# Performance work log

Measured on AMD Instinct MI355X. Metric: run time of the kernel, lower is better.

## Reference

```python
import math
import jax, jax.numpy as jnp
import numpy as np

B, N, DIM, H = 2, 4096, 1024, 16
DH = DIM // H
LEVELS = int(math.log2(N))
SCALE = 1.0 / math.sqrt(DH)


def build_lookup_table(seq_len):
    """Replicates build_hierarchical_index_lookup_table (numpy, static)."""
    levels = int(math.log2(seq_len))
    total_nodes = 2 * seq_len - 1
    max_valid = total_nodes - 2
    idx = np.full((seq_len, levels), -1, dtype=np.int32)
    cm = np.zeros((seq_len, levels), dtype=bool)
    for n in range(seq_len):
        nc = n
        for l in range(levels):
            if l == 0:
                pair = nc
                nn = nc ^ 1
            else:
                pair = nc // 2 + seq_len
                nn = pair ^ 1  # (nc//2 + seq_len) ^ 1 per Python precedence
            if nn > max_valid:
                break
            if pair < nn:
                cm[n, l] = True  # neighbor is to the right -> causally masked
            idx[n, l] = nn
            nc = nn
    return idx, cm


def setup_inputs() -> dict:
    key = jax.random.key(0)
    ks = jax.random.split(key, 12)
    w = lambda k: (jax.random.normal(k, (DIM, DIM), dtype=jnp.float32) * 0.02)
    idx_np, cm_np = build_lookup_table(N)
    return {
        "x": jax.random.normal(ks[0], (B, N, DIM), dtype=jnp.float32),
        "Wq_y": w(ks[1]), "Wk_y": w(ks[2]), "Wv_y": w(ks[3]),
        "Wo_y": w(ks[4]), "bo_y": jnp.zeros((DIM,), jnp.float32),
        "Wq_x": w(ks[5]), "Wk_x": w(ks[6]), "Wv_x": w(ks[7]),
        "Wo_x": w(ks[8]), "bo_x": jnp.zeros((DIM,), jnp.float32),
        "idx_map": jnp.asarray(idx_np, dtype=jnp.int32),       # [N, LEVELS]
        "causal_mask": jnp.asarray(cm_np, dtype=jnp.bool_),    # [N, LEVELS]
    }


def _heads(t):
    b, n, _ = t.shape
    return t.reshape(b, n, H, DH)


def _forward(x, Wq_y, Wk_y, Wv_y, Wo_y, bo_y, Wq_x, Wk_x, Wv_x, Wo_x, bo_x,
             idx_map, causal_mask):
    # ---- stage 1: build parent nodes level by level (online 2-child softmax merge)
    nodes = [x]  # leaves: [B, N, DIM]; parents appended level by level
    cur = x
    for _ in range(LEVELS):
        pre = 0.5 * (cur[:, 0::2] + cur[:, 1::2])     # parent query source [B,P,DIM]
        q = _heads(pre @ Wq_y)                        # [B,P,H,DH]
        k = _heads(cur @ Wk_y)                        # [B,C,H,DH]
        v = _heads(cur @ Wv_y)
        s0 = jnp.einsum('bphd,bphd->bph', q, k[:, 0::2]) * SCALE
        s1 = jnp.einsum('bphd,bphd->bph', q, k[:, 1::2]) * SCALE
        m = jnp.maximum(s0, s1)
        e0 = jnp.exp(s0 - m)
        e1 = jnp.exp(s1 - m)
        denom = e0 + e1 + 1e-9
        parent = ((e0 / denom)[..., None] * v[:, 0::2]
                  + (e1 / denom)[..., None] * v[:, 1::2])   # [B,P,H,DH]
        bp, pp = parent.shape[0], parent.shape[1]
        parent = parent.reshape(bp, pp, DIM) @ Wo_y + bo_y
        nodes.append(parent)
        cur = parent
    h_all = jnp.concatenate(nodes, axis=1)            # [B, 2N-1, DIM]

    # ---- stage 2: fused multi-level gather attention over self + neighbors
    Q = _heads(x @ Wq_x)                              # leaf queries [B,N,H,DH]
    K_all = _heads(h_all @ Wk_x)                      # [B,2N-1,H,DH]
    V_all = _heads(h_all @ Wv_x)

    k_cross = jnp.take(K_all, idx_map, axis=1)        # [B,N,LEVELS,H,DH]
    v_cross = jnp.take(V_all, idx_map, axis=1)

    s_self = jnp.einsum('bnhd,bnhd->bnh', Q, K_all[:, :N]) * SCALE   # [B,N,H]
    s_cross = jnp.einsum('bnhd,bnlhd->bnhl', Q, k_cross) * SCALE     # [B,N,H,L]
    neg_inf = jnp.float32(-jnp.inf)
    s_cross = jnp.where(causal_mask[None, :, None, :], neg_inf, s_cross)

    scores = jnp.concatenate([s_self[..., None], s_cross], axis=-1)  # [B,N,H,L+1]
    w = jax.nn.softmax(scores, axis=-1)
    out = (w[..., 0:1] * V_all[:, :N]
           + jnp.einsum('bnhl,bnlhd->bnhd', w[..., 1:], v_cross))    # [B,N,H,DH]
    return out.reshape(B, N, DIM) @ Wo_x + bo_x


def reference(x, Wq_y, Wk_y, Wv_y, Wo_y, bo_y, Wq_x, Wk_x, Wv_x, Wo_x, bo_x,
              idx_map, causal_mask):
    return _forward(x, Wq_y, Wk_y, Wv_y, Wo_y, bo_y,
                    Wq_x, Wk_x, Wv_x, Wo_x, bo_x, idx_map, causal_mask)
```

## Files before the change

### kernel.cpp

```cpp
#include <hip/hip_runtime.h>
#include <stdint.h>

#define H_NODES 8191
#define NN 4096
#define DIMC 1024

typedef __bf16 bf16x8 __attribute__((ext_vector_type(8)));
typedef float f32x4 __attribute__((ext_vector_type(4)));

__device__ __forceinline__ float b2f(ushort u) {
  union { uint32_t i; float f; } x; x.i = ((uint32_t)u) << 16; return x.f;
}
__device__ __forceinline__ ushort f2b(float f) {
  union { float f; uint32_t i; } x; x.f = f;
  uint32_t r = x.i + 0x7FFFu + ((x.i >> 16) & 1u);
  return (ushort)(r >> 16);
}
__device__ __forceinline__ void load16f(const ushort* p, float* f) {
  const uint32_t* w = (const uint32_t*)p;
  #pragma unroll
  for (int i = 0; i < 8; ++i) {
    uint32_t v = w[i];
    f[2 * i]     = b2f((ushort)(v & 0xffff));
    f[2 * i + 1] = b2f((ushort)(v >> 16));
  }
}
__device__ __forceinline__ void store16b(ushort* p, const float* f) {
  uint32_t w[8];
  #pragma unroll
  for (int i = 0; i < 8; ++i)
    w[i] = (uint32_t)f2b(f[2 * i]) | ((uint32_t)f2b(f[2 * i + 1]) << 16);
  *(uint4*)p = *(const uint4*)&w[0];
  *(uint4*)(p + 8) = *(const uint4*)&w[4];
}

struct WPtrs { const float* w[8]; };

__global__ void __launch_bounds__(256) transpose_w_k(WPtrs wp, ushort* __restrict__ dst) {
  __shared__ float t[32][33];
  const float* src = wp.w[blockIdx.z];
  int c0 = blockIdx.x * 32, r0 = blockIdx.y * 32;
  int tx = threadIdx.x, ty = threadIdx.y;
  #pragma unroll
  for (int i = ty; i < 32; i += 8)
    t[i][tx] = src[(long)(r0 + i) * DIMC + c0 + tx];
  __syncthreads();
  ushort* d = dst + (long)blockIdx.z * DIMC * DIMC;
  #pragma unroll
  for (int i = ty; i < 32; i += 8)
    d[(long)(c0 + i) * DIMC + r0 + tx] = f2b(t[tx][i]);
}

__global__ void __launch_bounds__(256) cvt_x_k(const float* __restrict__ x, ushort* __restrict__ h) {
  long t = (long)blockIdx.x * 256 + threadIdx.x;
  long i = t << 2;
  if (i >= (long)2 * NN * DIMC) return;
  long row = i >> 10;
  int col = (int)(i & 1023);
  long b = row >> 12;
  long n = row & 4095;
  float4 v = *(const float4*)(x + i);
  ushort* d = h + ((b * H_NODES + n) << 10) + col;
  uint2 pk;
  pk.x = (uint32_t)f2b(v.x) | ((uint32_t)f2b(v.y) << 16);
  pk.y = (uint32_t)f2b(v.z) | ((uint32_t)f2b(v.w) << 16);
  *(uint2*)d = pk;
}

__global__ void __launch_bounds__(256) avg_pairs_k(const ushort* __restrict__ h,
    ushort* __restrict__ pre, int P, int offL) {
  long t = (long)blockIdx.x * 256 + threadIdx.x;
  if (t >= (long)2 * P * 128) return;
  int dblk = (int)(t & 127);
  long r = t >> 7;
  int b = (r >= P) ? 1 : 0;
  int p = (int)(r - (long)b * P);
  const ushort* c = h + (((long)(b * H_NODES + offL + 2 * p)) << 10) + dblk * 8;
  const uint4 a0 = *(const uint4*)c;
  const uint4 a1 = *(const uint4*)(c + DIMC);
  const uint32_t* pa = (const uint32_t*)&a0;
  const uint32_t* pb = (const uint32_t*)&a1;
  uint32_t outw[4];
  #pragma unroll
  for (int i = 0; i < 4; ++i) {
    float x0 = b2f((ushort)(pa[i] & 0xffff)), x1 = b2f((ushort)(pa[i] >> 16));
    float y0 = b2f((ushort)(pb[i] & 0xffff)), y1 = b2f((ushort)(pb[i] >> 16));
    ushort r0 = f2b(0.5f * (x0 + y0)), r1 = f2b(0.5f * (x1 + y1));
    outw[i] = (uint32_t)r0 | ((uint32_t)r1 << 16);
  }
  *(uint4*)(pre + (((long)(b * P + p)) << 10) + dblk * 8) = *(const uint4*)outw;
}

struct GemmDesc {
  const ushort* A; long sAb;
  const ushort* Bt;
  const float* bias;
  void* C; long sCb; int ldc;
  int M; int outMode;
  int tX, tY;
  ushort* preC;
  long sPreB;
};

__device__ __forceinline__ void stage_tile(const GemmDesc& d, const ushort* Ab,
    int row0, int col0, ushort* lA, ushort* lB, int kt, int wave, int lane) {
  #pragma unroll
  for (int j = 0; j < 2; ++j) {
    int s = wave * 128 + j * 64 + lane;
    int r = s >> 2;
    int g = (s & 3) ^ ((r >> 1) & 3);
    int gr = row0 + r; gr = (gr < d.M) ? gr : (d.M - 1);
    const ushort* srcA = Ab + (long)gr * DIMC + kt * 32 + g * 8;
    __builtin_amdgcn_global_load_lds(
        (const __attribute__((address_space(1))) void*)(uintptr_t)srcA,
        (__attribute__((address_space(3))) void*)(uint32_t)(uintptr_t)(lA + (wave * 128 + j * 64) * 8),
        16, 0, 0);
    const ushort* srcB = d.Bt + (long)(col0 + r) * DIMC + kt * 32 + g * 8;
    __builtin_amdgcn_global_load_lds(
        (const __attribute__((address_space(1))) void*)(uintptr_t)srcB,
        (__attribute__((address_space(3))) void*)(uint32_t)(uintptr_t)(lB + (wave * 128 + j * 64) * 8),
        16, 0, 0);
  }
}

__device__ __forceinline__ void gemm_tile(const GemmDesc& d, int bz, int row0, int col0,
    ushort (*lA)[4096], ushort (*lB)[4096], int tid) {
  const ushort* Ab = d.A + (long)bz * d.sAb;
  int wave = tid >> 6, lane = tid & 63;
  int wr = wave >> 1, wc = wave & 1;

  f32x4 acc[4][4];
  #pragma unroll
  for (int m = 0; m < 4; ++m)
    #pragma unroll
    for (int n = 0; n < 4; ++n) acc[m][n] = (f32x4){0.f, 0.f, 0.f, 0.f};

  stage_tile(d, Ab, row0, col0, lA[0], lB[0], 0, wave, lane);
  stage_tile(d, Ab, row0, col0, lA[1], lB[1], 1, wave, lane);
  asm volatile("s_waitcnt vmcnt(4)" ::: "memory");
  __builtin_amdgcn_s_barrier();

  int rr = lane & 15, g4 = lane >> 4;
  for (int kt = 0; kt < 32; ++kt) {
    int cur = kt % 3;
    if (kt + 2 < 32)
      stage_tile(d, Ab, row0, col0, lA[(kt + 2) % 3], lB[(kt + 2) % 3], kt + 2, wave, lane);
    bf16x8 af[4], bfr[4];
    #pragma unroll
    for (int m = 0; m < 4; ++m) {
      int r = wr * 64 + m * 16 + rr;
      int slot = g4 ^ ((r >> 1) & 3);
      af[m] = *reinterpret_cast<const bf16x8*>(&lA[cur][r * 32 + slot * 8]);
    }
    #pragma unroll
    for (int n = 0; n < 4; ++n) {
      int r = wc * 64 + n * 16 + rr;
      int slot = g4 ^ ((r >> 1) & 3);
      bfr[n] = *reinterpret_cast<const bf16x8*>(&lB[cur][r * 32 + slot * 8]);
    }
    __builtin_amdgcn_s_setprio(1);
    #pragma unroll
    for (int m = 0; m < 4; ++m)
      #pragma unroll
      for (int n = 0; n < 4; ++n)
        acc[m][n] = __builtin_amdgcn_mfma_f32_16x16x32_bf16(af[m], bfr[n], acc[m][n], 0, 0, 0);
    __builtin_amdgcn_s_setprio(0);
    if (kt < 30) { asm volatile("s_waitcnt vmcnt(4)" ::: "memory"); }
    else         { asm volatile("s_waitcnt vmcnt(0)" ::: "memory"); }
    if (kt < 31) __builtin_amdgcn_s_barrier();
  }

  int rq = lane >> 4;
  #pragma unroll
  for (int n = 0; n < 4; ++n) {
    int col = col0 + wc * 64 + n * 16 + rr;
    float bv = d.bias ? d.bias[col] : 0.0f;
    #pragma unroll
    for (int m = 0; m < 4; ++m) {
      int gr0 = row0 + wr * 64 + m * 16 + rq * 4;
      float vv[4];
      #pragma unroll
      for (int r = 0; r < 4; ++r) vv[r] = acc[m][n][r] + bv;
      #pragma unroll
      for (int r = 0; r < 4; ++r) {
        int gr = gr0 + r;
        if (gr < d.M) {
          long o = (long)bz * d.sCb + (long)gr * d.ldc + col;
          if (d.outMode == 2) ((float*)d.C)[o] = vv[r];
          else ((ushort*)d.C)[o] = f2b(vv[r]);
        }
      }
      if (d.preC) {
        #pragma unroll
        for (int r = 0; r < 4; r += 2) {
          int gr = gr0 + r;
          if (gr + 1 < d.M)
            d.preC[(long)bz * d.sPreB + (long)(gr >> 1) * DIMC + col] =
                f2b(0.5f * (vv[r] + vv[r + 1]));
        }
      }
    }
  }
}

__global__ void __launch_bounds__(256) gemm_multi(GemmDesc d0, GemmDesc d1, int t0) {
  __shared__ __align__(16) ushort lA[3][4096];
  __shared__ __align__(16) ushort lB[3][4096];
  int t = blockIdx.x;
  const GemmDesc& d = (t < t0) ? d0 : d1;
  int u = (t < t0) ? t : t - t0;
  int per = d.tX * d.tY;
  int bz = u / per;
  int rem = u - bz * per;
  int ty = rem / d.tX;
  int tx = rem - ty * d.tX;
  gemm_tile(d, bz, tx * 128, ty * 128, lA, lB, threadIdx.x);
}

__global__ void __launch_bounds__(256) merge_y2_k(const ushort* __restrict__ q,
    const ushort* __restrict__ kv, ushort* __restrict__ outp, int P) {
  int wave = threadIdx.x >> 6, lane = threadIdx.x & 63;
  long w = (long)blockIdx.x * 4 + wave;
  if (w >= (long)2 * P) return;
  int b = (w >= P) ? 1 : 0;
  int p = (int)(w - (long)b * P);
  const ushort* qp = q + (((long)(b * P + p)) << 10) + lane * 16;
  const ushort* kvb = kv + ((long)(b * 2 * P + 2 * p)) * 2048;
  float qf[16], k0f[16], k1f[16];
  load16f(qp, qf);
  load16f(kvb + lane * 16, k0f);
  load16f(kvb + 2048 + lane * 16, k1f);
  float d0 = 0.f, d1 = 0.f;
  #pragma unroll
  for (int j = 0; j < 16; ++j) { d0 += qf[j] * k0f[j]; d1 += qf[j] * k1f[j]; }
  d0 += __shfl_xor(d0, 1); d0 += __shfl_xor(d0, 2);
  d1 += __shfl_xor(d1, 1); d1 += __shfl_xor(d1, 2);
  float s0 = d0 * 0.125f, s1 = d1 * 0.125f;
  float mm = fmaxf(s0, s1);
  float e0 = expf(s0 - mm), e1 = expf(s1 - mm);
  float inv = 1.0f / (e0 + e1 + 1e-9f);
  float w0 = e0 * inv, w1 = e1 * inv;
  float v0f[16], v1f[16], ov[16];
  load16f(kvb + 1024 + lane * 16, v0f);
  load16f(kvb + 2048 + 1024 + lane * 16, v1f);
  #pragma unroll
  for (int j = 0; j < 16; ++j) ov[j] = w0 * v0f[j] + w1 * v1f[j];
  store16b(outp + (((long)(b * P + p)) << 10) + lane * 16, ov);
}

__global__ void __launch_bounds__(256) attn_x2_k(const ushort* __restrict__ Q,
    const ushort* __restrict__ KV, ushort* __restrict__ outp) {
  int wave = threadIdx.x >> 6, lane = threadIdx.x & 63;
  long w = (long)blockIdx.x * 4 + wave;
  int n = (int)(w & 4095);
  int b = (int)(w >> 12);
  const ushort* KVb = KV + (long)b * H_NODES * 2048;
  float qf[16];
  load16f(Q + (((long)b * NN + n) << 10) + lane * 16, qf);
  int nb[13];
  nb[0] = n;
  #pragma unroll
  for (int l = 0; l < 12; ++l) nb[1 + l] = (8192 - (8192 >> l)) + ((n >> l) ^ 1);
  float s[13];
  #pragma unroll
  for (int i = 0; i < 13; ++i) {
    float kf[16];
    load16f(KVb + (long)nb[i] * 2048 + lane * 16, kf);
    float d = 0.f;
    #pragma unroll
    for (int j = 0; j < 16; ++j) d += qf[j] * kf[j];
    d += __shfl_xor(d, 1);
    d += __shfl_xor(d, 2);
    s[i] = d * 0.125f;
  }
  #pragma unroll
  for (int l = 0; l < 12; ++l)
    if (((n >> l) & 1) == 0) s[1 + l] = -__builtin_inff();
  float mm = s[0];
  #pragma unroll
  for (int i = 1; i < 13; ++i) mm = fmaxf(mm, s[i]);
  float e[13], sum = 0.f;
  #pragma unroll
  for (int i = 0; i < 13; ++i) { e[i] = expf(s[i] - mm); sum += e[i]; }
  float inv = 1.0f / sum;
  float ov[16];
  #pragma unroll
  for (int j = 0; j < 16; ++j) ov[j] = 0.f;
  #pragma unroll
  for (int i = 0; i < 13; ++i) {
    float wgt = e[i] * inv;
    float vf[16];
    load16f(KVb + (long)nb[i] * 2048 + 1024 + lane * 16, vf);
    #pragma unroll
    for (int j = 0; j < 16; ++j) ov[j] += wgt * vf[j];
  }
  store16b(outp + (((long)b * NN + n) << 10) + lane * 16, ov);
}

extern "C" void kernel_launch(void* const* d_in, const int* in_sizes, int n_in,
                              void* d_out, int out_size, void* d_ws, size_t ws_size,
                              hipStream_t stream) {
  const float* x    = (const float*)d_in[0];
  const float* Wq_y = (const float*)d_in[1];
  const float* Wk_y = (const float*)d_in[2];
  const float* Wv_y = (const float*)d_in[3];
  const float* Wo_y = (const float*)d_in[4];
  const float* bo_y = (const float*)d_in[5];
  const float* Wq_x = (const float*)d_in[6];
  const float* Wk_x = (const float*)d_in[7];
  const float* Wv_x = (const float*)d_in[8];
  const float* Wo_x = (const float*)d_in[9];
  const float* bo_x = (const float*)d_in[10];

  ushort* wt  = (ushort*)d_ws;
  ushort* h   = wt + (size_t)8 * 1024 * 1024;
  ushort* reg = h + (size_t)2 * H_NODES * DIMC;
  ushort* Qx   = reg;
  ushort* KVa  = Qx + (size_t)2 * 4096 * DIMC;
  ushort* aout = KVa + (size_t)2 * H_NODES * 2048;
  ushort* preB = reg;
  ushort* qbB  = preB + (size_t)2 * 2048 * DIMC;
  ushort* kv1B = qbB + (size_t)2 * 2048 * DIMC;
  ushort* mrgB = kv1B + (size_t)2 * 4096 * 2048;
  ushort* preS = aout;
  ushort* qbS  = preS + (size_t)2 * 256 * DIMC;
  ushort* kv1S = qbS + (size_t)2 * 256 * DIMC;
  ushort* mrgS = kv1S + (size_t)2 * 512 * 2048;

  size_t need = ((size_t)8 * 1024 * 1024 + (size_t)2 * H_NODES * DIMC +
                 (size_t)2 * 4096 * DIMC + (size_t)2 * H_NODES * 2048 +
                 (size_t)2 * 4096 * DIMC) * 2;
  if (ws_size < need) return;

  WPtrs wp;
  wp.w[0] = Wq_y; wp.w[1] = Wk_y; wp.w[2] = Wv_y; wp.w[3] = Wo_y;
  wp.w[4] = Wq_x; wp.w[5] = Wk_x; wp.w[6] = Wv_x; wp.w[7] = Wo_x;
  transpose_w_k<<<dim3(32, 32, 8), dim3(32, 8), 0, stream>>>(wp, wt);
  cvt_x_k<<<8192, 256, 0, stream>>>(x, h);
  avg_pairs_k<<<(2 * 2048 * 128 + 255) / 256, 256, 0, stream>>>(h, preB, 2048, 0);

  auto mk128 = [](const ushort* A, long sAb, const ushort* Bt, const float* bias,
                  void* C, long sCb, int ldc, int M, int outMode, int tY) {
    GemmDesc d; d.A = A; d.sAb = sAb; d.Bt = Bt; d.bias = bias; d.C = C; d.sCb = sCb;
    d.ldc = ldc; d.M = M; d.outMode = outMode; d.tX = (M + 127) / 128; d.tY = tY;
    d.preC = nullptr; d.sPreB = 0;
    return d;
  };
  auto kvSub = [&](long start, int len) {
    return mk128(h + start * DIMC, (long)H_NODES * DIMC, wt + (size_t)5 * 1024 * 1024,
                 nullptr, KVa + start * 2048, (long)H_NODES * 2048, 2048, len, 0, 16);
  };

  for (int l = 0; l < 12; ++l) {
    int P = NN >> (l + 1);
    int offL = 8192 - (8192 >> l);
    int offP = 8192 - (8192 >> (l + 1));
    bool small = (l >= 3);
    ushort* pre = small ? preS : preB;
    ushort* qb  = small ? qbS  : qbB;
    ushort* kv1 = small ? kv1S : kv1B;
    ushort* mrg = small ? mrgS : mrgB;

    GemmDesc dq  = mk128(pre, (long)P * DIMC, wt, nullptr,
                         qb, (long)P * DIMC, DIMC, P, 0, 8);
    GemmDesc dkv = mk128(h + (long)offL * DIMC, (long)H_NODES * DIMC,
                         wt + (size_t)1 * 1024 * 1024, nullptr,
                         kv1, (long)2 * P * 2048, 2048, 2 * P, 0, 16);
    int t0 = dq.tX * dq.tY * 2;
    gemm_multi<<<t0 + dkv.tX * dkv.tY * 2, 256, 0, stream>>>(dq, dkv, t0);

    merge_y2_k<<<(2 * P + 3) / 4, 256, 0, stream>>>(qb, kv1, mrg, P);

    GemmDesc dgo = mk128(mrg, (long)P * DIMC, wt + (size_t)3 * 1024 * 1024, bo_y,
                         h + (long)offP * DIMC, (long)H_NODES * DIMC, DIMC, P, 1, 8);
    if (l < 11) {
      dgo.preC = (l >= 2) ? preS : preB;
      dgo.sPreB = (long)(P / 2) * DIMC;
    }
    GemmDesc att = dgo; int nAtt = 0;
    if (l == 4)      { att = kvSub(0, 2048); }
    else if (l == 5) { att = kvSub(2048, 2048); }
    else if (l == 6) { att = kvSub(4096, 2048); }
    else if (l == 7) { att = kvSub(6144, 1792); }
    else if (l == 8) { att = kvSub(7936, 240); }
    else if (l == 9) { att = mk128(h, (long)H_NODES * DIMC, wt + (size_t)4 * 1024 * 1024,
                                   nullptr, Qx, (long)4096 * DIMC, DIMC, 4096, 0, 8); }
    else if (l == 10) { att = kvSub(8176, 12); }
    else if (l == 11) { att = kvSub(8188, 2); }
    if (l >= 4) nAtt = att.tX * att.tY * 2;
    int n0 = dgo.tX * dgo.tY * 2;
    gemm_multi<<<n0 + nAtt, 256, 0, stream>>>(dgo, att, n0);
  }

  {
    GemmDesc att = kvSub(8190, 1);
    gemm_multi<<<att.tX * att.tY * 2, 256, 0, stream>>>(att, att, att.tX * att.tY * 2);
  }
  attn_x2_k<<<2048, 256, 0, stream>>>(Qx, KVa, aout);
  {
    GemmDesc dox = mk128(aout, (long)4096 * DIMC, wt + (size_t)7 * 1024 * 1024, bo_x,
                         d_out, (long)4096 * DIMC, DIMC, 4096, 2, 8);
    gemm_multi<<<dox.tX * dox.tY * 2, 256, 0, stream>>>(dox, dox, dox.tX * dox.tY * 2);
  }
}
```

Before: 661.3 us.

## Redistribute attention K/V and Q projection GEMMs across more level launches

```diff
diff --git a/kernel.cpp b/kernel.cpp
--- a/kernel.cpp
+++ b/kernel.cpp
@@ -203,12 +203,13 @@
   }
 }
 
-__global__ void __launch_bounds__(256) gemm_multi(GemmDesc d0, GemmDesc d1, int t0) {
+__global__ void __launch_bounds__(256) gemm_multi(GemmDesc d0, GemmDesc d1, GemmDesc d2,
+                                                  int t0, int t1) {
   __shared__ __align__(16) ushort lA[3][4096];
   __shared__ __align__(16) ushort lB[3][4096];
   int t = blockIdx.x;
-  const GemmDesc& d = (t < t0) ? d0 : d1;
-  int u = (t < t0) ? t : t - t0;
+  const GemmDesc& d = (t < t0) ? d0 : ((t < t1) ? d1 : d2);
+  int u = (t < t0) ? t : ((t < t1) ? t - t0 : t - t1);
   int per = d.tX * d.tY;
   int bz = u / per;
   int rem = u - bz * per;
@@ -350,6 +351,9 @@
     return mk128(h + start * DIMC, (long)H_NODES * DIMC, wt + (size_t)5 * 1024 * 1024,
                  nullptr, KVa + start * 2048, (long)H_NODES * 2048, 2048, len, 0, 16);
   };
+  auto tiles = [](const GemmDesc& d) { return d.tX * d.tY * 2; };
+  GemmDesc dQat = mk128(h, (long)H_NODES * DIMC, wt + (size_t)4 * 1024 * 1024, nullptr,
+                        Qx, (long)4096 * DIMC, DIMC, 4096, 0, 8);
 
   for (int l = 0; l < 12; ++l) {
     int P = NN >> (l + 1);
@@ -366,8 +370,18 @@
     GemmDesc dkv = mk128(h + (long)offL * DIMC, (long)H_NODES * DIMC,
                          wt + (size_t)1 * 1024 * 1024, nullptr,
                          kv1, (long)2 * P * 2048, 2048, 2 * P, 0, 16);
-    int t0 = dq.tX * dq.tY * 2;
-    gemm_multi<<<t0 + dkv.tX * dkv.tY * 2, 256, 0, stream>>>(dq, dkv, t0);
+    GemmDesc aq = dkv; int naq = 0;
+    if      (l == 4)  { aq = kvSub(1024, 1024); }
+    else if (l == 5)  { aq = kvSub(4096, 1024); }
+    else if (l == 6)  { aq = kvSub(6144, 1024); }
+    else if (l == 7)  { aq = kvSub(8128, 32); }
+    else if (l == 8)  { aq = kvSub(8160, 16); }
+    else if (l == 9)  { aq = kvSub(8176, 8); }
+    else if (l == 10) { aq = kvSub(8184, 4); }
+    else if (l == 11) { aq = kvSub(8188, 2); }
+    if (l >= 4) naq = tiles(aq);
+    int nq = tiles(dq), nkv = tiles(dkv);
+    gemm_multi<<<nq + nkv + naq, 256, 0, stream>>>(dq, dkv, aq, nq, nq + nkv);
 
     merge_y2_k<<<(2 * P + 3) / 4, 256, 0, stream>>>(qb, kv1, mrg, P);
 
@@ -377,29 +391,27 @@
       dgo.preC = (l >= 2) ? preS : preB;
       dgo.sPreB = (long)(P / 2) * DIMC;
     }
-    GemmDesc att = dgo; int nAtt = 0;
-    if (l == 4)      { att = kvSub(0, 2048); }
-    else if (l == 5) { att = kvSub(2048, 2048); }
-    else if (l == 6) { att = kvSub(4096, 2048); }
-    else if (l == 7) { att = kvSub(6144, 1792); }
-    else if (l == 8) { att = kvSub(7936, 240); }
-    else if (l == 9) { att = mk128(h, (long)H_NODES * DIMC, wt + (size_t)4 * 1024 * 1024,
-                                   nullptr, Qx, (long)4096 * DIMC, DIMC, 4096, 0, 8); }
-    else if (l == 10) { att = kvSub(8176, 12); }
-    else if (l == 11) { att = kvSub(8188, 2); }
-    if (l >= 4) nAtt = att.tX * att.tY * 2;
-    int n0 = dgo.tX * dgo.tY * 2;
-    gemm_multi<<<n0 + nAtt, 256, 0, stream>>>(dgo, att, n0);
+    GemmDesc a1 = dgo, a2 = dgo; int n1 = 0, n2 = 0;
+    if      (l == 3) { a1 = kvSub(0, 1024); n1 = tiles(a1); }
+    else if (l == 4) { a1 = kvSub(2048, 1024); a2 = kvSub(3072, 1024);
+                       n1 = tiles(a1); n2 = tiles(a2); }
+    else if (l == 5) { a1 = dQat; a2 = kvSub(5120, 1024);
+                       n1 = tiles(a1); n2 = tiles(a2); }
+    else if (l == 6) { a1 = kvSub(7168, 960); n1 = tiles(a1); }
+    int n0 = tiles(dgo);
+    gemm_multi<<<n0 + n1 + n2, 256, 0, stream>>>(dgo, a1, a2, n0, n0 + n1);
   }
 
   {
     GemmDesc att = kvSub(8190, 1);
-    gemm_multi<<<att.tX * att.tY * 2, 256, 0, stream>>>(att, att, att.tX * att.tY * 2);
+    int n = tiles(att);
+    gemm_multi<<<n, 256, 0, stream>>>(att, att, att, n, n);
   }
   attn_x2_k<<<2048, 256, 0, stream>>>(Qx, KVa, aout);
   {
     GemmDesc dox = mk128(aout, (long)4096 * DIMC, wt + (size_t)7 * 1024 * 1024, bo_x,
                          d_out, (long)4096 * DIMC, DIMC, 4096, 2, 8);
-    gemm_multi<<<dox.tX * dox.tY * 2, 256, 0, stream>>>(dox, dox, dox.tX * dox.tY * 2);
-  }
-}
+    int n = tiles(dox);
+    gemm_multi<<<n, 256, 0, stream>>>(dox, dox, dox, n, n);
+  }
+}
```

Measured after the change: 924.6 us. 39.8% more time.

## Rebalance Qx/KV projection GEMMs across tree levels and unify scratch buffers

Applied to the files above, without the earlier changes.

```diff
diff --git a/kernel.cpp b/kernel.cpp
--- a/kernel.cpp
+++ b/kernel.cpp
@@ -318,19 +318,21 @@
   ushort* Qx   = reg;
   ushort* KVa  = Qx + (size_t)2 * 4096 * DIMC;
   ushort* aout = KVa + (size_t)2 * H_NODES * 2048;
-  ushort* preB = reg;
+  ushort* preB = aout;
   ushort* qbB  = preB + (size_t)2 * 2048 * DIMC;
+  ushort* mrgQ = qbB;
   ushort* kv1B = qbB + (size_t)2 * 2048 * DIMC;
   ushort* mrgB = kv1B + (size_t)2 * 4096 * 2048;
-  ushort* preS = aout;
-  ushort* qbS  = preS + (size_t)2 * 256 * DIMC;
-  ushort* kv1S = qbS + (size_t)2 * 256 * DIMC;
-  ushort* mrgS = kv1S + (size_t)2 * 512 * 2048;
-
-  size_t need = ((size_t)8 * 1024 * 1024 + (size_t)2 * H_NODES * DIMC +
-                 (size_t)2 * 4096 * DIMC + (size_t)2 * H_NODES * 2048 +
-                 (size_t)2 * 4096 * DIMC) * 2;
-  if (ws_size < need) return;
+  ushort* preS = preB;
+  ushort* qbS  = qbB;
+  ushort* kv1S = kv1B;
+  ushort* mrgS = mrgB;
+
+  size_t wsElems = (size_t)8 * 1024 * 1024 + (size_t)2 * H_NODES * DIMC +
+                   (size_t)2 * 4096 * DIMC + (size_t)2 * H_NODES * 2048 +
+                   ((size_t)2 * 2048 * DIMC * 2 + (size_t)2 * 4096 * 2048 +
+                    (size_t)2 * 2048 * DIMC);
+  if (ws_size < wsElems * 2) return;
 
   WPtrs wp;
   wp.w[0] = Wq_y; wp.w[1] = Wk_y; wp.w[2] = Wv_y; wp.w[3] = Wo_y;
@@ -350,16 +352,19 @@
     return mk128(h + start * DIMC, (long)H_NODES * DIMC, wt + (size_t)5 * 1024 * 1024,
                  nullptr, KVa + start * 2048, (long)H_NODES * 2048, 2048, len, 0, 16);
   };
+  auto qSub = [&](long start, int len) {
+    return mk128(h + start * DIMC, (long)H_NODES * DIMC, wt + (size_t)4 * 1024 * 1024,
+                 nullptr, Qx + start * DIMC, (long)4096 * DIMC, DIMC, len, 0, 8);
+  };
 
   for (int l = 0; l < 12; ++l) {
     int P = NN >> (l + 1);
     int offL = 8192 - (8192 >> l);
     int offP = 8192 - (8192 >> (l + 1));
-    bool small = (l >= 3);
-    ushort* pre = small ? preS : preB;
-    ushort* qb  = small ? qbS  : qbB;
-    ushort* kv1 = small ? kv1S : kv1B;
-    ushort* mrg = small ? mrgS : mrgB;
+    ushort* pre = (l >= 3) ? preS : preB;
+    ushort* qb  = (l >= 3) ? qbS  : qbB;
+    ushort* kv1 = (l >= 3) ? kv1S : kv1B;
+    ushort* mrg = (l >= 3) ? mrgS : mrgB;
 
     GemmDesc dq  = mk128(pre, (long)P * DIMC, wt, nullptr,
                          qb, (long)P * DIMC, DIMC, P, 0, 8);
@@ -378,23 +383,27 @@
       dgo.sPreB = (long)(P / 2) * DIMC;
     }
     GemmDesc att = dgo; int nAtt = 0;
-    if (l == 4)      { att = kvSub(0, 2048); }
-    else if (l == 5) { att = kvSub(2048, 2048); }
-    else if (l == 6) { att = kvSub(4096, 2048); }
-    else if (l == 7) { att = kvSub(6144, 1792); }
-    else if (l == 8) { att = kvSub(7936, 240); }
-    else if (l == 9) { att = mk128(h, (long)H_NODES * DIMC, wt + (size_t)4 * 1024 * 1024,
-                                   nullptr, Qx, (long)4096 * DIMC, DIMC, 4096, 0, 8); }
-    else if (l == 10) { att = kvSub(8176, 12); }
-    else if (l == 11) { att = kvSub(8188, 2); }
-    if (l >= 4) nAtt = att.tX * att.tY * 2;
+    if      (l == 0)  att = qSub(0, 2048);
+    else if (l == 1)  att = qSub(2048, 2048);
+    else if (l == 2)  att = kvSub(0, 1792);
+    else if (l == 3)  att = kvSub(1792, 1920);
+    else if (l == 4)  att = kvSub(3712, 1920);
+    else if (l == 5)  att = kvSub(5632, 1536);
+    else if (l == 6)  att = kvSub(7168, 512);
+    else if (l == 7)  att = kvSub(7680, 256);
+    else if (l == 8)  att = kvSub(7936, 128);
+    else if (l == 9)  att = kvSub(8064, 64);
+    else if (l == 10) att = kvSub(8128, 32);
+    else if (l == 11) att = kvSub(8160, 16);
+    nAtt = att.tX * att.tY * 2;
     int n0 = dgo.tX * dgo.tY * 2;
     gemm_multi<<<n0 + nAtt, 256, 0, stream>>>(dgo, att, n0);
   }
 
   {
-    GemmDesc att = kvSub(8190, 1);
-    gemm_multi<<<att.tX * att.tY * 2, 256, 0, stream>>>(att, att, att.tX * att.tY * 2);
+    GemmDesc a0 = kvSub(8176, 8), a1 = kvSub(8184, 7);
+    int n0 = a0.tX * a0.tY * 2, n1 = a1.tX * a1.tY * 2;
+    gemm_multi<<<n0 + n1, 256, 0, stream>>>(a0, a1, n0);
   }
   attn_x2_k<<<2048, 256, 0, stream>>>(Qx, KVa, aout);
   {
```

Result: no change. 649.6 us (-1.8%).
